# Optimization experiments

Measured on AMD Instinct MI355X. Metric: run time of the kernel, lower is better.

The kernel has to match this reference:

```python
import jax, jax.numpy as jnp
import numpy as np

IMG_SIZES = [56, 28, 14, 7]


def setup_inputs() -> dict:
    key = jax.random.key(0)
    k0, k1, k2, k3, kp = jax.random.split(key, 5)
    return {
        "feat0": jax.random.normal(k0, (8, 64, 56, 56), dtype=jnp.float32),
        "feat1": jax.random.normal(k1, (8, 128, 28, 28), dtype=jnp.float32),
        "feat2": jax.random.normal(k2, (8, 256, 14, 14), dtype=jnp.float32),
        "feat3": jax.random.normal(k3, (8, 512, 7, 7), dtype=jnp.float32),
        "pts": jax.random.normal(kp, (131072, 3), dtype=jnp.float32),
        "batch": 3,
    }


def _project(feat, h, w, size):
    # feat: [C, size, size]; h, w: [N] float in [0, 223]
    x = h / (224.0 / size)
    y = w / (224.0 / size)
    x1 = jnp.floor(x).astype(jnp.int32)
    x2 = jnp.minimum(jnp.ceil(x).astype(jnp.int32), size - 1)
    y1 = jnp.floor(y).astype(jnp.int32)
    y2 = jnp.minimum(jnp.ceil(y).astype(jnp.int32), size - 1)
    # NOTE: original casts x,y to long BEFORE computing weights (truncation),
    # so weights are integer 0/1 -- reproduced faithfully.
    xl = x.astype(jnp.int32)
    yl = y.astype(jnp.int32)
    g = lambda xi, yi: feat[:, xi, yi].T  # [N, C] gather
    w11 = ((x2 - xl) * (y2 - yl)).astype(feat.dtype)[:, None]
    w12 = ((x2 - xl) * (yl - y1)).astype(feat.dtype)[:, None]
    w21 = ((xl - x1) * (y2 - yl)).astype(feat.dtype)[:, None]
    w22 = ((xl - x1) * (yl - y1)).astype(feat.dtype)[:, None]
    return w11 * g(x1, y1) + w21 * g(x2, y1) + w12 * g(x1, y2) + w22 * g(x2, y2)


def reference(feat0, feat1, feat2, feat3, pts, batch):
    h = 248.0 * (pts[:, 1] / pts[:, 2]) + 111.5
    w = 248.0 * (pts[:, 0] / (-pts[:, 2])) + 111.5
    h = jnp.clip(h, 0.0, 223.0)
    w = jnp.clip(w, 0.0, 223.0)
    feats = [feat0[batch], feat1[batch], feat2[batch], feat3[batch]]
    outs = [_project(f, h, w, s) for f, s in zip(feats, IMG_SIZES)]
    return jnp.concatenate(outs, axis=1)  # [N, 960]
```

## Files before the change

kernel.cpp:

```cpp
#include <hip/hip_runtime.h>

#define NPTS 131072
#define FT_TOTAL 376320

typedef float f32x4 __attribute__((ext_vector_type(4)));

__global__ __launch_bounds__(256) void k_prep(
    const float* __restrict__ pts,
    int4* __restrict__ idx4,
    const float* __restrict__ f0,
    const float* __restrict__ f1,
    const float* __restrict__ f2,
    const float* __restrict__ f3,
    const int* __restrict__ batch,
    float* __restrict__ ft)
{
    int blk = blockIdx.x;
    if (blk < 512) {
        int n = blk * 256 + threadIdx.x;
        float px = pts[3 * n + 0];
        float py = pts[3 * n + 1];
        float pz = pts[3 * n + 2];
        float qh = __fdiv_rn(py, pz);
        float qw = __fdiv_rn(px, -pz);
        float h = __fadd_rn(__fmul_rn(248.0f, qh), 111.5f);
        float w = __fadd_rn(__fmul_rn(248.0f, qw), 111.5f);
        h = fminf(fmaxf(h, 0.0f), 223.0f);
        w = fminf(fmaxf(w, 0.0f), 223.0f);

        const float scl[4] = {0.25f, 0.125f, 0.0625f, 0.03125f};
        const int   S[4]   = {56, 28, 14, 7};
        int r[4];
#pragma unroll
        for (int s = 0; s < 4; ++s) {
            float x = h * scl[s];
            float y = w * scl[s];
            int x1 = (int)floorf(x);
            int x2 = min((int)ceilf(x), S[s] - 1);
            int y1 = (int)floorf(y);
            int y2 = min((int)ceilf(y), S[s] - 1);
            int bit = (x2 - x1) * (y2 - y1);
            r[s] = bit ? (x1 * S[s] + y1) : -1;
        }
        idx4[n] = make_int4(r[0], r[1], r[2], r[3]);
    } else {
        int d = (blk - 512) * 256 + threadIdx.x;
        int b = *batch;
        const float* src;
        int local, c, p, hw;
        if (d < 200704) {
            local = d;          c = local & 63;  p = local >> 6; hw = 3136;
            src = f0 + (size_t)b * 64 * 3136;
        } else if (d < 301056) {
            local = d - 200704; c = local & 127; p = local >> 7; hw = 784;
            src = f1 + (size_t)b * 128 * 784;
        } else if (d < 351232) {
            local = d - 301056; c = local & 255; p = local >> 8; hw = 196;
            src = f2 + (size_t)b * 256 * 196;
        } else {
            local = d - 351232; c = local & 511; p = local >> 9; hw = 49;
            src = f3 + (size_t)b * 512 * 49;
        }
        ft[d] = src[c * hw + p];
    }
}

__global__ __launch_bounds__(256) void k_gather(
    const int* __restrict__ idx,
    const float* __restrict__ ft,
    float* __restrict__ out)
{
    int gid = blockIdx.x * 256 + threadIdx.x;
    int n = gid / 240;
    int j = gid - n * 240;

    int s, C, toff, cb;
    if (j < 16)       { s = 0; C = 64;  toff = 0;      cb = j * 4; }
    else if (j < 48)  { s = 1; C = 128; toff = 200704; cb = (j - 16) * 4; }
    else if (j < 112) { s = 2; C = 256; toff = 301056; cb = (j - 48) * 4; }
    else              { s = 3; C = 512; toff = 351232; cb = (j - 112) * 4; }

    int id = idx[n * 4 + s];
    f32x4 v = (f32x4)(0.0f);
    if (id >= 0) {
        v = *(const f32x4*)(ft + toff + id * C + cb);
    }
    *(f32x4*)(out + (size_t)n * 960 + j * 4) = v;
}

extern "C" void kernel_launch(void* const* d_in, const int* in_sizes, int n_in,
                              void* d_out, int out_size, void* d_ws, size_t ws_size,
                              hipStream_t stream) {
    const float* f0  = (const float*)d_in[0];
    const float* f1  = (const float*)d_in[1];
    const float* f2  = (const float*)d_in[2];
    const float* f3  = (const float*)d_in[3];
    const float* pts = (const float*)d_in[4];
    const int* batch = (const int*)d_in[5];

    int4* idx4 = (int4*)d_ws;
    float* ft = (float*)((char*)d_ws + (size_t)NPTS * 16);
    float* out = (float*)d_out;

    k_prep<<<512 + 1470, 256, 0, stream>>>(pts, idx4, f0, f1, f2, f3, batch, ft);
    k_gather<<<122880, 256, 0, stream>>>((const int*)idx4, ft, out);
}
```

Measured before the change: 497.6 us.

## Fuse projection, transpose and gather into a single kernel

Removes the prep kernel that computed per-point indices and transposed the feature maps into channel-last layout. The single kernel now recomputes the projection per thread (240 threads per point) and gathers four strided channel values straight from the original NCHW feature maps. This saves one launch and the workspace round trip, but adds redundant divisions per thread and uncoalesced strided loads in place of a single 16-byte vector load.

```diff
diff --git a/kernel.cpp b/kernel.cpp
--- a/kernel.cpp
+++ b/kernel.cpp
@@ -1,91 +1,58 @@
 #include <hip/hip_runtime.h>
 
 #define NPTS 131072
-#define FT_TOTAL 376320
 
 typedef float f32x4 __attribute__((ext_vector_type(4)));
 
-__global__ __launch_bounds__(256) void k_prep(
+__global__ __launch_bounds__(256) void k_fused(
     const float* __restrict__ pts,
-    int4* __restrict__ idx4,
     const float* __restrict__ f0,
     const float* __restrict__ f1,
     const float* __restrict__ f2,
     const float* __restrict__ f3,
     const int* __restrict__ batch,
-    float* __restrict__ ft)
-{
-    int blk = blockIdx.x;
-    if (blk < 512) {
-        int n = blk * 256 + threadIdx.x;
-        float px = pts[3 * n + 0];
-        float py = pts[3 * n + 1];
-        float pz = pts[3 * n + 2];
-        float qh = __fdiv_rn(py, pz);
-        float qw = __fdiv_rn(px, -pz);
-        float h = __fadd_rn(__fmul_rn(248.0f, qh), 111.5f);
-        float w = __fadd_rn(__fmul_rn(248.0f, qw), 111.5f);
-        h = fminf(fmaxf(h, 0.0f), 223.0f);
-        w = fminf(fmaxf(w, 0.0f), 223.0f);
-
-        const float scl[4] = {0.25f, 0.125f, 0.0625f, 0.03125f};
-        const int   S[4]   = {56, 28, 14, 7};
-        int r[4];
-#pragma unroll
-        for (int s = 0; s < 4; ++s) {
-            float x = h * scl[s];
-            float y = w * scl[s];
-            int x1 = (int)floorf(x);
-            int x2 = min((int)ceilf(x), S[s] - 1);
-            int y1 = (int)floorf(y);
-            int y2 = min((int)ceilf(y), S[s] - 1);
-            int bit = (x2 - x1) * (y2 - y1);
-            r[s] = bit ? (x1 * S[s] + y1) : -1;
-        }
-        idx4[n] = make_int4(r[0], r[1], r[2], r[3]);
-    } else {
-        int d = (blk - 512) * 256 + threadIdx.x;
-        int b = *batch;
-        const float* src;
-        int local, c, p, hw;
-        if (d < 200704) {
-            local = d;          c = local & 63;  p = local >> 6; hw = 3136;
-            src = f0 + (size_t)b * 64 * 3136;
-        } else if (d < 301056) {
-            local = d - 200704; c = local & 127; p = local >> 7; hw = 784;
-            src = f1 + (size_t)b * 128 * 784;
-        } else if (d < 351232) {
-            local = d - 301056; c = local & 255; p = local >> 8; hw = 196;
-            src = f2 + (size_t)b * 256 * 196;
-        } else {
-            local = d - 351232; c = local & 511; p = local >> 9; hw = 49;
-            src = f3 + (size_t)b * 512 * 49;
-        }
-        ft[d] = src[c * hw + p];
-    }
-}
-
-__global__ __launch_bounds__(256) void k_gather(
-    const int* __restrict__ idx,
-    const float* __restrict__ ft,
     float* __restrict__ out)
 {
     int gid = blockIdx.x * 256 + threadIdx.x;
     int n = gid / 240;
     int j = gid - n * 240;
 
-    int s, C, toff, cb;
-    if (j < 16)       { s = 0; C = 64;  toff = 0;      cb = j * 4; }
-    else if (j < 48)  { s = 1; C = 128; toff = 200704; cb = (j - 16) * 4; }
-    else if (j < 112) { s = 2; C = 256; toff = 301056; cb = (j - 48) * 4; }
-    else              { s = 3; C = 512; toff = 351232; cb = (j - 112) * 4; }
+    int s, S, HW, cb;
+    const float* fsrc;
+    float scl;
+    if (j < 16)       { s = 0; S = 56; HW = 3136; cb = j * 4;         fsrc = f0; scl = 0.25f;    }
+    else if (j < 48)  { s = 1; S = 28; HW = 784;  cb = (j - 16) * 4;  fsrc = f1; scl = 0.125f;   }
+    else if (j < 112) { s = 2; S = 14; HW = 196;  cb = (j - 48) * 4;  fsrc = f2; scl = 0.0625f;  }
+    else              { s = 3; S = 7;  HW = 49;   cb = (j - 112) * 4; fsrc = f3; scl = 0.03125f; }
 
-    int id = idx[n * 4 + s];
+    float px = pts[3 * n + 0];
+    float py = pts[3 * n + 1];
+    float pz = pts[3 * n + 2];
+    float qh = __fdiv_rn(py, pz);
+    float qw = __fdiv_rn(px, -pz);
+    float h = __fadd_rn(__fmul_rn(248.0f, qh), 111.5f);
+    float w = __fadd_rn(__fmul_rn(248.0f, qw), 111.5f);
+    h = fminf(fmaxf(h, 0.0f), 223.0f);
+    w = fminf(fmaxf(w, 0.0f), 223.0f);
+
+    float x = h * scl;
+    float y = w * scl;
+    int x1 = (int)floorf(x);
+    int x2 = min((int)ceilf(x), S - 1);
+    int y1 = (int)floorf(y);
+    int y2 = min((int)ceilf(y), S - 1);
+    int bit = (x2 - x1) * (y2 - y1);
+
     f32x4 v = (f32x4)(0.0f);
-    if (id >= 0) {
-        v = *(const f32x4*)(ft + toff + id * C + cb);
+    if (bit) {
+        int b = *batch;
+        const float* g = fsrc + ((b * (64 << s) + cb) * HW + x1 * S + y1);
+        v.x = g[0];
+        v.y = g[HW];
+        v.z = g[2 * HW];
+        v.w = g[3 * HW];
     }
-    *(f32x4*)(out + (size_t)n * 960 + j * 4) = v;
+    *((f32x4*)out + gid) = v;
 }
 
 extern "C" void kernel_launch(void* const* d_in, const int* in_sizes, int n_in,
@@ -97,11 +64,7 @@
     const float* f3  = (const float*)d_in[3];
     const float* pts = (const float*)d_in[4];
     const int* batch = (const int*)d_in[5];
-
-    int4* idx4 = (int4*)d_ws;
-    float* ft = (float*)((char*)d_ws + (size_t)NPTS * 16);
     float* out = (float*)d_out;
 
-    k_prep<<<512 + 1470, 256, 0, stream>>>(pts, idx4, f0, f1, f2, f3, batch, ft);
-    k_gather<<<122880, 256, 0, stream>>>((const int*)idx4, ft, out);
+    k_fused<<<122880, 256, 0, stream>>>(pts, f0, f1, f2, f3, batch, out);
 }
```

Measured after the change: 560.1 us. 12.6% more time.
